# Performance work log

Measured on AMD Instinct MI355X. Metric: run time of the kernel, lower is better.

Reference implementation:

```python
import jax, jax.numpy as jnp
import numpy as np

C, H, W = 3, 128, 128
N_PIX = C * H * W            # 49152
N_RET = N_PIX // 16          # 3072
N_LGN = N_RET                # 3072
N_V1 = 2 * N_RET             # 6144
N_IT = N_RET                 # 3072
N_CLS = 1000
BATCH = 256


def setup_inputs() -> dict:
    key = jax.random.key(0)
    ks = jax.random.split(key, 14)
    x = jax.random.normal(ks[0], (BATCH, C, H, W), dtype=jnp.float32)
    w_ret = jax.random.normal(ks[1], (N_RET, 16), dtype=jnp.float32) * 0.1
    b_ret = jax.random.normal(ks[2], (N_RET,), dtype=jnp.float32) * 0.1
    w_lgn = jax.random.normal(ks[3], (N_LGN, 16), dtype=jnp.float32) * 0.1
    b_lgn = jax.random.normal(ks[4], (N_LGN,), dtype=jnp.float32) * 0.1
    w_v1 = jax.random.normal(ks[5], (N_V1, 32), dtype=jnp.float32) * 0.1
    b_v1 = jax.random.normal(ks[6], (N_V1,), dtype=jnp.float32) * 0.1
    w_it = jax.random.normal(ks[7], (N_IT, 32), dtype=jnp.float32) * 0.1
    b_it = jax.random.normal(ks[8], (N_IT,), dtype=jnp.float32) * 0.1
    W_cls = jax.random.normal(ks[9], (N_CLS, N_IT), dtype=jnp.float32) * 0.02
    b_cls = jnp.zeros((N_CLS,), dtype=jnp.float32)
    # pixel_map: arange(n_pixels) tiled/truncated to (n_retina, 16); here exact reshape
    pixel_map = jnp.arange(N_PIX, dtype=jnp.int32).reshape(N_RET, 16)
    m1 = jax.random.bernoulli(ks[10], 0.01, (N_V1, N_LGN)).astype(jnp.int32)
    m1 = m1.at[jnp.arange(N_V1), jnp.arange(N_V1) % N_LGN].set(1)
    m2 = jax.random.bernoulli(ks[11], 0.01, (N_IT, N_V1)).astype(jnp.int32)
    m2 = m2.at[jnp.arange(N_IT), jnp.arange(N_IT) % N_V1].set(1)
    return {"x": x, "w_ret": w_ret, "b_ret": b_ret, "w_lgn": w_lgn, "b_lgn": b_lgn,
            "w_v1": w_v1, "b_v1": b_v1, "w_it": w_it, "b_it": b_it,
            "W_cls": W_cls, "b_cls": b_cls, "pixel_map": pixel_map,
            "lgn_to_v1": m1, "v1_to_it": m2}


def reference(x, w_ret, b_ret, w_lgn, b_lgn, w_v1, b_v1, w_it, b_it,
              W_cls, b_cls, pixel_map, lgn_to_v1, v1_to_it):
    B = x.shape[0]
    x_flat = x.reshape(B, -1)                                  # [B, n_pix]
    # Retina: per-neuron gather of 16-pixel receptive field, then spike
    pix = x_flat[:, pixel_map.reshape(-1)].reshape(B, N_RET, 16)  # [B, n_ret, 16]
    r1 = jax.nn.sigmoid(jnp.einsum('bnk,nk->bn', pix, w_ret) - b_ret)
    # LGN: scalar input broadcast over the 4x4 field -> scalar * sum(w)
    r2 = jax.nn.sigmoid(r1 * jnp.sum(w_lgn, axis=1) - b_lgn)
    # V1: mean over sparse LGN neighborhood, broadcast over 4x8 field
    m1 = lgn_to_v1.astype(r2.dtype)                             # [n_v1, n_lgn]
    v1_in = (r2 @ m1.T) / jnp.sum(m1, axis=1)                   # [B, n_v1]
    r3 = jax.nn.sigmoid(v1_in * jnp.sum(w_v1, axis=1) - b_v1)
    # IT: mean over sparse V1 neighborhood
    m2 = v1_to_it.astype(r3.dtype)                              # [n_it, n_v1]
    it_in = (r3 @ m2.T) / jnp.sum(m2, axis=1)                   # [B, n_it]
    r4 = jax.nn.sigmoid(it_in * jnp.sum(w_it, axis=1) - b_it)
    return r4 @ W_cls.T + b_cls                                 # [B, n_classes]
```

## Files before the change

### kernel.cpp

```cpp
#include <hip/hip_runtime.h>

#define B     256
#define NPIX  49152
#define NRET  3072
#define NV1   6144
#define NIT   3072
#define NCLS  1000

typedef unsigned short ushort_t;
typedef __bf16 bf16x8 __attribute__((ext_vector_type(8)));
typedef float  f32x4  __attribute__((ext_vector_type(4)));
typedef int    i32x4  __attribute__((ext_vector_type(4)));

__device__ __forceinline__ float sigmoidf_(float v) {
    return 1.0f / (1.0f + __expf(-v));
}

__device__ __forceinline__ ushort_t f2bf(float f) {
    union { float f; unsigned u; } v; v.f = f;
    unsigned r = (v.u + 0x7fffu + ((v.u >> 16) & 1u)) >> 16;
    return (ushort_t)r;
}

__global__ __launch_bounds__(256) void k_retina_t(
    const float* __restrict__ x, const float* __restrict__ w_ret,
    const float* __restrict__ b_ret, const float* __restrict__ w_lgn,
    const float* __restrict__ b_lgn, const int* __restrict__ pixel_map,
    float* __restrict__ r2t)
{
    __shared__ float tile[32][33];
    int tx = threadIdx.x & 31, ty = threadIdx.x >> 5;
    int n0 = blockIdx.x * 32, b0 = blockIdx.y * 32;
    int n = n0 + tx;
    const int4*   pm4 = (const int4*)(pixel_map + n * 16);
    const float4* wr4 = (const float4*)(w_ret + n * 16);
    const float4* wl4 = (const float4*)(w_lgn + n * 16);
    int4 p[4]; float4 wr[4]; float slw = 0.f;
#pragma unroll
    for (int q = 0; q < 4; ++q) {
        p[q] = pm4[q]; wr[q] = wr4[q];
        float4 L = wl4[q]; slw += L.x + L.y + L.z + L.w;
    }
    float br = b_ret[n], bl = b_lgn[n];
#pragma unroll
    for (int i = 0; i < 4; ++i) {
        int b = b0 + ty + i * 8;
        const float* xb = x + (size_t)b * NPIX;
        float dot = 0.f;
#pragma unroll
        for (int q = 0; q < 4; ++q)
            dot += xb[p[q].x] * wr[q].x + xb[p[q].y] * wr[q].y
                 + xb[p[q].z] * wr[q].z + xb[p[q].w] * wr[q].w;
        float r1 = sigmoidf_(dot - br);
        tile[ty + i * 8][tx] = sigmoidf_(r1 * slw - bl);
    }
    __syncthreads();
#pragma unroll
    for (int i = 0; i < 4; ++i)
        r2t[(size_t)(n0 + ty + i * 8) * B + b0 + tx] = tile[tx][ty + i * 8];
}

template<int K, bool OUT_BF16>
__global__ __launch_bounds__(256) void k_sparse(
    const float* __restrict__ act_t,
    const int*   __restrict__ mask,
    const float* __restrict__ w,
    const float* __restrict__ bias,
    void*        __restrict__ out_t)
{
    constexpr int MAXI = 192;
    __shared__ int idxs[4][MAXI];
    int t = threadIdx.x, wv = t >> 6, l = t & 63;
    int j = blockIdx.x * 4 + wv;

    const i32x4* row4 = (const i32x4*)(mask + (size_t)j * K);
    int cnt = 0;
#pragma unroll
    for (int it = 0; it < K / 256; ++it) {
        int q = it * 64 + l;
        i32x4 m = __builtin_nontemporal_load(&row4[q]);
        int base = q * 4;
#pragma unroll
        for (int f = 0; f < 4; ++f) {
            int mv = m[f];
            unsigned long long bal = __ballot(mv != 0);
            int pre = __builtin_amdgcn_mbcnt_hi((unsigned)(bal >> 32),
                      __builtin_amdgcn_mbcnt_lo((unsigned)bal, 0));
            int slot = cnt + pre;
            if (mv && slot < MAXI) idxs[wv][slot] = base + f;
            cnt += __popcll(bal);
        }
    }
    int n = cnt < MAXI ? cnt : MAXI;

    const float4* a4 = (const float4*)act_t;
    float4 acc0 = {0,0,0,0}, acc1 = {0,0,0,0}, acc2 = {0,0,0,0}, acc3 = {0,0,0,0};
    int i = 0;
    for (; i + 4 <= n; i += 4) {
        int j0 = idxs[wv][i], j1 = idxs[wv][i + 1];
        int j2 = idxs[wv][i + 2], j3 = idxs[wv][i + 3];
        float4 v0 = a4[(size_t)j0 * 64 + l];
        float4 v1 = a4[(size_t)j1 * 64 + l];
        float4 v2 = a4[(size_t)j2 * 64 + l];
        float4 v3 = a4[(size_t)j3 * 64 + l];
        acc0.x += v0.x; acc0.y += v0.y; acc0.z += v0.z; acc0.w += v0.w;
        acc1.x += v1.x; acc1.y += v1.y; acc1.z += v1.z; acc1.w += v1.w;
        acc2.x += v2.x; acc2.y += v2.y; acc2.z += v2.z; acc2.w += v2.w;
        acc3.x += v3.x; acc3.y += v3.y; acc3.z += v3.z; acc3.w += v3.w;
    }
    for (; i < n; ++i) {
        float4 v0 = a4[(size_t)idxs[wv][i] * 64 + l];
        acc0.x += v0.x; acc0.y += v0.y; acc0.z += v0.z; acc0.w += v0.w;
    }
    acc0.x += acc1.x + acc2.x + acc3.x;
    acc0.y += acc1.y + acc2.y + acc3.y;
    acc0.z += acc1.z + acc2.z + acc3.z;
    acc0.w += acc1.w + acc2.w + acc3.w;

    float sw = w[(size_t)j * 32 + (l & 31)];
#pragma unroll
    for (int off = 1; off < 32; off <<= 1) sw += __shfl_xor(sw, off);

    float bj = bias[j];
    float scale = sw / (float)n;
    float o0 = sigmoidf_(acc0.x * scale - bj);
    float o1 = sigmoidf_(acc0.y * scale - bj);
    float o2 = sigmoidf_(acc0.z * scale - bj);
    float o3 = sigmoidf_(acc0.w * scale - bj);

    if (OUT_BF16) {
        ushort_t* dst = (ushort_t*)out_t + (size_t)j * B + l * 4;
        ushort4 o; o.x = f2bf(o0); o.y = f2bf(o1); o.z = f2bf(o2); o.w = f2bf(o3);
        *(ushort4*)dst = o;
    } else {
        float4* dst = (float4*)((float*)out_t + (size_t)j * B + l * 4);
        float4 o; o.x = o0; o.y = o1; o.z = o2; o.w = o3;
        *dst = o;
    }
}

__global__ __launch_bounds__(256) void k_prep(
    const float* __restrict__ W,
    const ushort_t* __restrict__ r4bt,
    ushort_t* __restrict__ wbf,
    ushort_t* __restrict__ r4b)
{
    __shared__ ushort_t stile[32][33];
    int bx = blockIdx.x, t = threadIdx.x;
    if (bx < 1536) {
        int e = (bx * 256 + t) * 8;
        uint4 o = {0, 0, 0, 0};
        if (e < NCLS * NIT) {
            float4 f0 = *(const float4*)(W + e);
            float4 f1 = *(const float4*)(W + e + 4);
            o.x = (unsigned)f2bf(f0.x) | ((unsigned)f2bf(f0.y) << 16);
            o.y = (unsigned)f2bf(f0.z) | ((unsigned)f2bf(f0.w) << 16);
            o.z = (unsigned)f2bf(f1.x) | ((unsigned)f2bf(f1.y) << 16);
            o.w = (unsigned)f2bf(f1.z) | ((unsigned)f2bf(f1.w) << 16);
        }
        *(uint4*)(wbf + e) = o;
    } else {
        int tb = bx - 1536;
        int tn = tb / 8, tbb = tb % 8;
        int tx = t & 31, ty = t >> 5;
#pragma unroll
        for (int i = 0; i < 4; ++i)
            stile[ty + i * 8][tx] = r4bt[(size_t)(tn * 32 + ty + i * 8) * B + tbb * 32 + tx];
        __syncthreads();
#pragma unroll
        for (int i = 0; i < 4; ++i)
            r4b[(size_t)(tbb * 32 + ty + i * 8) * NIT + tn * 32 + tx] = stile[tx][ty + i * 8];
    }
}

__global__ __launch_bounds__(256) void k_cls_mfma(
    const ushort_t* __restrict__ r4b,
    const ushort_t* __restrict__ wbf,
    float* __restrict__ part)
{
    int t = threadIdx.x, wv = t >> 6, l = t & 63;
    int cb = blockIdx.x, bb = blockIdx.y, kz = blockIdx.z;
    int m = l & 15, quad = l >> 4;
    int brow = bb * 64 + wv * 16 + m;
    const bf16x8* pa = (const bf16x8*)(r4b + (size_t)brow * NIT + kz * 768 + quad * 8);
    const bf16x8* pb0 = (const bf16x8*)(wbf + (size_t)(cb * 64 +  0 + m) * NIT + kz * 768 + quad * 8);
    const bf16x8* pb1 = (const bf16x8*)(wbf + (size_t)(cb * 64 + 16 + m) * NIT + kz * 768 + quad * 8);
    const bf16x8* pb2 = (const bf16x8*)(wbf + (size_t)(cb * 64 + 32 + m) * NIT + kz * 768 + quad * 8);
    const bf16x8* pb3 = (const bf16x8*)(wbf + (size_t)(cb * 64 + 48 + m) * NIT + kz * 768 + quad * 8);

    f32x4 acc0 = {0,0,0,0}, acc1 = {0,0,0,0}, acc2 = {0,0,0,0}, acc3 = {0,0,0,0};
#pragma unroll 4
    for (int s = 0; s < 24; ++s) {
        bf16x8 a  = pa [s * 4];
        bf16x8 b0 = pb0[s * 4];
        bf16x8 b1 = pb1[s * 4];
        bf16x8 b2 = pb2[s * 4];
        bf16x8 b3 = pb3[s * 4];
        acc0 = __builtin_amdgcn_mfma_f32_16x16x32_bf16(a, b0, acc0, 0, 0, 0);
        acc1 = __builtin_amdgcn_mfma_f32_16x16x32_bf16(a, b1, acc1, 0, 0, 0);
        acc2 = __builtin_amdgcn_mfma_f32_16x16x32_bf16(a, b2, acc2, 0, 0, 0);
        acc3 = __builtin_amdgcn_mfma_f32_16x16x32_bf16(a, b3, acc3, 0, 0, 0);
    }
    float* dst = part + (size_t)kz * (B * NCLS);
    int rb = bb * 64 + wv * 16 + quad * 4;
#pragma unroll
    for (int ct = 0; ct < 4; ++ct) {
        f32x4 a = ct == 0 ? acc0 : ct == 1 ? acc1 : ct == 2 ? acc2 : acc3;
        int c = cb * 64 + ct * 16 + m;
        if (c < NCLS) {
#pragma unroll
            for (int r = 0; r < 4; ++r)
                dst[(size_t)(rb + r) * NCLS + c] = a[r];
        }
    }
}

__global__ __launch_bounds__(256) void k_reduce(
    const float* __restrict__ part, const float* __restrict__ b_cls,
    float* __restrict__ out)
{
    int i = blockIdx.x * 256 + threadIdx.x;
    float s = b_cls[i % NCLS];
#pragma unroll
    for (int z = 0; z < 4; ++z) s += part[(size_t)z * (B * NCLS) + i];
    out[i] = s;
}

extern "C" void kernel_launch(void* const* d_in, const int* in_sizes, int n_in,
                              void* d_out, int out_size, void* d_ws, size_t ws_size,
                              hipStream_t stream) {
    const float* x      = (const float*)d_in[0];
    const float* w_ret  = (const float*)d_in[1];
    const float* b_ret  = (const float*)d_in[2];
    const float* w_lgn  = (const float*)d_in[3];
    const float* b_lgn  = (const float*)d_in[4];
    const float* w_v1   = (const float*)d_in[5];
    const float* b_v1   = (const float*)d_in[6];
    const float* w_it   = (const float*)d_in[7];
    const float* b_it   = (const float*)d_in[8];
    const float* W_cls  = (const float*)d_in[9];
    const float* b_cls  = (const float*)d_in[10];
    const int*   pixmap = (const int*)d_in[11];
    const int*   m1     = (const int*)d_in[12];
    const int*   m2     = (const int*)d_in[13];
    float* out = (float*)d_out;

    char* w = (char*)d_ws;
    float*    r2t  = (float*)(w);
    float*    r3t  = (float*)(w +  3145728);
    ushort_t* r4bt = (ushort_t*)(w +  9437184);
    ushort_t* r4b  = (ushort_t*)(w + 11010048);
    ushort_t* wbf  = (ushort_t*)(w + 12582912);
    float*    part = (float*)(w + 18874368);

    k_retina_t<<<dim3(NRET / 32, B / 32), 256, 0, stream>>>(
        x, w_ret, b_ret, w_lgn, b_lgn, pixmap, r2t);
    k_sparse<NRET, false><<<NV1 / 4, 256, 0, stream>>>(r2t, m1, w_v1, b_v1, r3t);
    k_sparse<NV1, true><<<NIT / 4, 256, 0, stream>>>(r3t, m2, w_it, b_it, r4bt);
    k_prep<<<2304, 256, 0, stream>>>(W_cls, r4bt, wbf, r4b);
    k_cls_mfma<<<dim3(16, 4, 4), 256, 0, stream>>>(r4b, wbf, part);
    k_reduce<<<(B * NCLS) / 256, 256, 0, stream>>>(part, b_cls, out);
}
```

Baseline: 287.6 us.

## Store intermediate activations as bf16 and batch mask loads in sparse kernels

Retina and V1 activations are now written as bf16 instead of fp32, which halves the gather traffic in both sparse-mean kernels. Each wave now gathers two rows at once, one per 32-lane half, using 16-byte loads, and combines the halves with a shuffle. The mask scan issues twelve nontemporal loads up front before running the ballot compaction, to keep more memory requests in flight. This adds bf16 rounding to intermediate activations, and the mask loop assumes K is a multiple of 3072.

```diff
diff --git a/kernel.cpp b/kernel.cpp
--- a/kernel.cpp
+++ b/kernel.cpp
@@ -22,13 +22,25 @@
     return (ushort_t)r;
 }
 
+__device__ __forceinline__ void bfacc(uint4 v, float* acc) {
+    unsigned u0 = v.x, u1 = v.y, u2 = v.z, u3 = v.w;
+    acc[0] += __uint_as_float(u0 << 16);
+    acc[1] += __uint_as_float(u0 & 0xffff0000u);
+    acc[2] += __uint_as_float(u1 << 16);
+    acc[3] += __uint_as_float(u1 & 0xffff0000u);
+    acc[4] += __uint_as_float(u2 << 16);
+    acc[5] += __uint_as_float(u2 & 0xffff0000u);
+    acc[6] += __uint_as_float(u3 << 16);
+    acc[7] += __uint_as_float(u3 & 0xffff0000u);
+}
+
 __global__ __launch_bounds__(256) void k_retina_t(
     const float* __restrict__ x, const float* __restrict__ w_ret,
     const float* __restrict__ b_ret, const float* __restrict__ w_lgn,
     const float* __restrict__ b_lgn, const int* __restrict__ pixel_map,
-    float* __restrict__ r2t)
-{
-    __shared__ float tile[32][33];
+    ushort_t* __restrict__ r2t)
+{
+    __shared__ ushort_t tile[32][33];
     int tx = threadIdx.x & 31, ty = threadIdx.x >> 5;
     int n0 = blockIdx.x * 32, b0 = blockIdx.y * 32;
     int n = n0 + tx;
@@ -52,7 +64,7 @@
             dot += xb[p[q].x] * wr[q].x + xb[p[q].y] * wr[q].y
                  + xb[p[q].z] * wr[q].z + xb[p[q].w] * wr[q].w;
         float r1 = sigmoidf_(dot - br);
-        tile[ty + i * 8][tx] = sigmoidf_(r1 * slw - bl);
+        tile[ty + i * 8][tx] = f2bf(sigmoidf_(r1 * slw - bl));
     }
     __syncthreads();
 #pragma unroll
@@ -60,62 +72,73 @@
         r2t[(size_t)(n0 + ty + i * 8) * B + b0 + tx] = tile[tx][ty + i * 8];
 }
 
-template<int K, bool OUT_BF16>
+template<int K>
 __global__ __launch_bounds__(256) void k_sparse(
-    const float* __restrict__ act_t,
-    const int*   __restrict__ mask,
-    const float* __restrict__ w,
-    const float* __restrict__ bias,
-    void*        __restrict__ out_t)
+    const ushort_t* __restrict__ act_t,
+    const int*      __restrict__ mask,
+    const float*    __restrict__ w,
+    const float*    __restrict__ bias,
+    ushort_t*       __restrict__ out_t)
 {
     constexpr int MAXI = 192;
     __shared__ int idxs[4][MAXI];
     int t = threadIdx.x, wv = t >> 6, l = t & 63;
+    int half = l >> 5, lb = l & 31;
     int j = blockIdx.x * 4 + wv;
 
     const i32x4* row4 = (const i32x4*)(mask + (size_t)j * K);
     int cnt = 0;
 #pragma unroll
-    for (int it = 0; it < K / 256; ++it) {
-        int q = it * 64 + l;
-        i32x4 m = __builtin_nontemporal_load(&row4[q]);
-        int base = q * 4;
-#pragma unroll
-        for (int f = 0; f < 4; ++f) {
-            int mv = m[f];
-            unsigned long long bal = __ballot(mv != 0);
-            int pre = __builtin_amdgcn_mbcnt_hi((unsigned)(bal >> 32),
-                      __builtin_amdgcn_mbcnt_lo((unsigned)bal, 0));
-            int slot = cnt + pre;
-            if (mv && slot < MAXI) idxs[wv][slot] = base + f;
-            cnt += __popcll(bal);
+    for (int h = 0; h < K / 3072; ++h) {
+        i32x4 mb[12];
+#pragma unroll
+        for (int it = 0; it < 12; ++it)
+            mb[it] = __builtin_nontemporal_load(&row4[h * 768 + it * 64 + l]);
+#pragma unroll
+        for (int it = 0; it < 12; ++it) {
+            int base = (h * 768 + it * 64 + l) * 4;
+#pragma unroll
+            for (int f = 0; f < 4; ++f) {
+                int mv = mb[it][f];
+                unsigned long long bal = __ballot(mv != 0);
+                int pre = __builtin_amdgcn_mbcnt_hi((unsigned)(bal >> 32),
+                          __builtin_amdgcn_mbcnt_lo((unsigned)bal, 0));
+                int slot = cnt + pre;
+                if (mv && slot < MAXI) idxs[wv][slot] = base + f;
+                cnt += __popcll(bal);
+            }
         }
     }
     int n = cnt < MAXI ? cnt : MAXI;
 
-    const float4* a4 = (const float4*)act_t;
-    float4 acc0 = {0,0,0,0}, acc1 = {0,0,0,0}, acc2 = {0,0,0,0}, acc3 = {0,0,0,0};
+    const uint4* a4 = (const uint4*)act_t;
+    float acc[8] = {0,0,0,0,0,0,0,0};
+    float acc2[8] = {0,0,0,0,0,0,0,0};
     int i = 0;
-    for (; i + 4 <= n; i += 4) {
-        int j0 = idxs[wv][i], j1 = idxs[wv][i + 1];
-        int j2 = idxs[wv][i + 2], j3 = idxs[wv][i + 3];
-        float4 v0 = a4[(size_t)j0 * 64 + l];
-        float4 v1 = a4[(size_t)j1 * 64 + l];
-        float4 v2 = a4[(size_t)j2 * 64 + l];
-        float4 v3 = a4[(size_t)j3 * 64 + l];
-        acc0.x += v0.x; acc0.y += v0.y; acc0.z += v0.z; acc0.w += v0.w;
-        acc1.x += v1.x; acc1.y += v1.y; acc1.z += v1.z; acc1.w += v1.w;
-        acc2.x += v2.x; acc2.y += v2.y; acc2.z += v2.z; acc2.w += v2.w;
-        acc3.x += v3.x; acc3.y += v3.y; acc3.z += v3.z; acc3.w += v3.w;
-    }
-    for (; i < n; ++i) {
-        float4 v0 = a4[(size_t)idxs[wv][i] * 64 + l];
-        acc0.x += v0.x; acc0.y += v0.y; acc0.z += v0.z; acc0.w += v0.w;
-    }
-    acc0.x += acc1.x + acc2.x + acc3.x;
-    acc0.y += acc1.y + acc2.y + acc3.y;
-    acc0.z += acc1.z + acc2.z + acc3.z;
-    acc0.w += acc1.w + acc2.w + acc3.w;
+    int n4 = n & ~3;
+    for (; i < n4; i += 4) {
+        int ja = idxs[wv][i + half];
+        int jb = idxs[wv][i + 2 + half];
+        uint4 va = a4[(size_t)ja * 32 + lb];
+        uint4 vb = a4[(size_t)jb * 32 + lb];
+        bfacc(va, acc);
+        bfacc(vb, acc2);
+    }
+    if (i + 2 <= n) {
+        uint4 va = a4[(size_t)idxs[wv][i + half] * 32 + lb];
+        bfacc(va, acc);
+        i += 2;
+    }
+    if (n & 1) {
+        if (half == 0) {
+            uint4 va = a4[(size_t)idxs[wv][n - 1] * 32 + lb];
+            bfacc(va, acc);
+        }
+    }
+#pragma unroll
+    for (int k = 0; k < 8; ++k) acc[k] += acc2[k];
+#pragma unroll
+    for (int k = 0; k < 8; ++k) acc[k] += __shfl_xor(acc[k], 32);
 
     float sw = w[(size_t)j * 32 + (l & 31)];
 #pragma unroll
@@ -123,19 +146,17 @@
 
     float bj = bias[j];
     float scale = sw / (float)n;
-    float o0 = sigmoidf_(acc0.x * scale - bj);
-    float o1 = sigmoidf_(acc0.y * scale - bj);
-    float o2 = sigmoidf_(acc0.z * scale - bj);
-    float o3 = sigmoidf_(acc0.w * scale - bj);
-
-    if (OUT_BF16) {
-        ushort_t* dst = (ushort_t*)out_t + (size_t)j * B + l * 4;
-        ushort4 o; o.x = f2bf(o0); o.y = f2bf(o1); o.z = f2bf(o2); o.w = f2bf(o3);
-        *(ushort4*)dst = o;
-    } else {
-        float4* dst = (float4*)((float*)out_t + (size_t)j * B + l * 4);
-        float4 o; o.x = o0; o.y = o1; o.z = o2; o.w = o3;
-        *dst = o;
+    if (half == 0) {
+        uint4 o;
+        unsigned r[8];
+#pragma unroll
+        for (int k = 0; k < 8; ++k)
+            r[k] = f2bf(sigmoidf_(acc[k] * scale - bj));
+        o.x = r[0] | (r[1] << 16);
+        o.y = r[2] | (r[3] << 16);
+        o.z = r[4] | (r[5] << 16);
+        o.w = r[6] | (r[7] << 16);
+        *(uint4*)(out_t + (size_t)j * B + lb * 8) = o;
     }
 }
 
@@ -246,17 +267,17 @@
     float* out = (float*)d_out;
 
     char* w = (char*)d_ws;
-    float*    r2t  = (float*)(w);
-    float*    r3t  = (float*)(w +  3145728);
-    ushort_t* r4bt = (ushort_t*)(w +  9437184);
-    ushort_t* r4b  = (ushort_t*)(w + 11010048);
-    ushort_t* wbf  = (ushort_t*)(w + 12582912);
-    float*    part = (float*)(w + 18874368);
+    ushort_t* r2t  = (ushort_t*)(w);
+    ushort_t* r3t  = (ushort_t*)(w +  1572864);
+    ushort_t* r4bt = (ushort_t*)(w +  4718592);
+    ushort_t* r4b  = (ushort_t*)(w +  6291456);
+    ushort_t* wbf  = (ushort_t*)(w +  7864320);
+    float*    part = (float*)(w + 14155776);
 
     k_retina_t<<<dim3(NRET / 32, B / 32), 256, 0, stream>>>(
         x, w_ret, b_ret, w_lgn, b_lgn, pixmap, r2t);
-    k_sparse<NRET, false><<<NV1 / 4, 256, 0, stream>>>(r2t, m1, w_v1, b_v1, r3t);
-    k_sparse<NV1, true><<<NIT / 4, 256, 0, stream>>>(r3t, m2, w_it, b_it, r4bt);
+    k_sparse<NRET><<<NV1 / 4, 256, 0, stream>>>(r2t, m1, w_v1, b_v1, r3t);
+    k_sparse<NV1><<<NIT / 4, 256, 0, stream>>>(r3t, m2, w_it, b_it, r4bt);
     k_prep<<<2304, 256, 0, stream>>>(W_cls, r4bt, wbf, r4b);
     k_cls_mfma<<<dim3(16, 4, 4), 256, 0, stream>>>(r4b, wbf, part);
     k_reduce<<<(B * NCLS) / 256, 256, 0, stream>>>(part, b_cls, out);
```

Result: faster. 276.5 us (-3.8%).
